# Optimization experiments

Hardware: AMD Instinct MI355X
Metric: run time of the kernel (lower is better)

The kernel has to match this reference:

```python
import jax, jax.numpy as jnp
import numpy as np

T, P, E, H = 200000, 100000, 600000, 256

def setup_inputs() -> dict:
    key = jax.random.key(0)
    ks = jax.random.split(key, 8)
    x = jax.random.normal(ks[0], (T, H), dtype=jnp.float32)
    points = jax.random.normal(ks[1], (P, 3), dtype=jnp.float32)
    triangles = jax.random.randint(ks[2], (T, 3), 0, P)
    triangle_edges = jax.random.randint(ks[3], (2, E), 0, T)
    din = H + 9
    W1 = jax.random.normal(ks[4], (din, H), dtype=jnp.float32) / np.sqrt(din)
    b1 = jnp.zeros((H,), dtype=jnp.float32)
    W2 = jax.random.normal(ks[5], (H, H), dtype=jnp.float32) / np.sqrt(H)
    b2 = jnp.zeros((H,), dtype=jnp.float32)
    return {"x": x, "points": points, "triangles": triangles,
            "triangle_edges": triangle_edges, "W1": W1, "b1": b1, "W2": W2, "b2": b2}

def reference(x, points, triangles, triangle_edges, W1, b1, W2, b2):
    # Per-triangle geometry: [T, 3(corners), 3(xyz)]
    tp = points[triangles]
    e_ij = tp[:, 0] - tp[:, 1]
    e_ik = tp[:, 0] - tp[:, 2]
    e_jk = tp[:, 1] - tp[:, 2]
    edge_vectors = jnp.stack([e_ij, e_ik, e_jk], axis=1)  # [T,3,3]
    t_max = jnp.max(edge_vectors, axis=1).astype(x.dtype)  # [T,3]
    t_min = jnp.min(edge_vectors, axis=1).astype(x.dtype)  # [T,3]
    barycenters = jnp.mean(tp, axis=1).astype(x.dtype)     # [T,3]

    src = triangle_edges[0]
    tgt = triangle_edges[1]
    # Relative geometric descriptor per edge: [E, 9]
    r_n_k = jnp.concatenate([t_min[src] - t_min[tgt],
                             t_max[src] - t_max[tgt],
                             barycenters[src] - barycenters[tgt]], axis=1)
    feature_diff = x[src] - x[tgt]                          # [E, H]
    mlp_in = jnp.concatenate([r_n_k, feature_diff], axis=1)  # [E, H+9]
    h = jax.nn.relu(mlp_in @ W1 + b1)
    mlp_out = h @ W2 + b2                                   # [E, H]
    # Scatter-add back to source triangles (order-independent sum)
    new_features = jax.ops.segment_sum(mlp_out, src, num_segments=x.shape[0])
    return new_features.astype(x.dtype)
```

## Files before the change

kernel.cpp:

```cpp
#include <hip/hip_runtime.h>
#include <stdint.h>

typedef float f32x4v __attribute__((ext_vector_type(4)));
typedef short short8v __attribute__((ext_vector_type(8)));

__device__ __forceinline__ float bf2f(unsigned short u) {
  union { uint32_t i; float f; } v; v.i = ((uint32_t)u) << 16; return v.f;
}
__device__ __forceinline__ unsigned short f2bf(float f) {
  union { float f; uint32_t i; } v; v.f = f;
  uint32_t x = v.i;
  uint32_t r = (x + 0x7FFFu + ((x >> 16) & 1u)) >> 16;
  return (unsigned short)r;
}

__global__ void prep_weights(const float* __restrict__ W1, const float* __restrict__ W2,
                             unsigned short* __restrict__ W1fT, unsigned short* __restrict__ W2T) {
  int i = blockIdx.x * blockDim.x + threadIdx.x;
  if (i < 256 * 288) {
    int n = i / 288, k = i % 288;
    float v = 0.f;
    if (k < 256) v = W1[(9 + k) * 256 + n];
    else if (k < 265) v = W1[(k - 256) * 256 + n];
    W1fT[i] = f2bf(v);
// ... 81 lines not shown
  int wbase = 0;
#pragma unroll
  for (int w = 0; w < 4; ++w) if (w < wave) wbase += wsums[w];
  if (tid < nb) blockbase[tid] = wbase + inclv - v;
}

__global__ void scan3_kernel(const int* __restrict__ count, const int* __restrict__ incl,
                             const int* __restrict__ blockbase, int* __restrict__ offsets,
                             int* __restrict__ cursor, int T) {
  int idx = blockIdx.x * 1024 + threadIdx.x * 4;
  int bb = blockbase[blockIdx.x];
#pragma unroll
  for (int j = 0; j < 4; ++j) {
    int i = idx + j;
    if (i < T) {
      int o = incl[i] + bb;
      offsets[i + 1] = o;
      cursor[i] = o - count[i];
    }
  }
  if (blockIdx.x == 0 && threadIdx.x == 0) offsets[0] = 0;
}

__global__ void fill_kernel(const int* __restrict__ te, int* __restrict__ cursor,
                            int* __restrict__ tgt_list, int E) {
  int e = blockIdx.x * blockDim.x + threadIdx.x;
  if (e < E) {
    int s = te[e];
    int pos = atomicAdd(&cursor[s], 1);
    tgt_list[pos] = te[E + e];
  }
}

__launch_bounds__(256)
__global__ void ugemm_kernel(const float* __restrict__ x, const float* __restrict__ geo12,
                             const unsigned short* __restrict__ W1fT,
                             unsigned short* __restrict__ U, int T) {
  __shared__ alignas(16) unsigned short Al[2][64][40];
  int m0 = blockIdx.x * 64;
  int tid = threadIdx.x;
  int wid = tid >> 6, lane = tid & 63;
  int srow = tid >> 2, cq = tid & 3;
  int l15 = lane & 15, lhi = lane >> 4;
  int nbase = wid * 64;
  f32x4v acc[4][4] = {};
  const unsigned short* bp[4];
#pragma unroll
  for (int nf = 0; nf < 4; ++nf)
    bp[nf] = W1fT + (size_t)(nbase + nf * 16 + l15) * 288 + 8 * lhi;
  int t = m0 + srow;

  auto loadf = [&](int kk, float* f) {
    if (kk < 8) {
      const float* sp = x + (size_t)t * 256 + kk * 32 + cq * 8;
      float4 a = *(const float4*)sp;
      float4 b = *(const float4*)(sp + 4);
      f[0] = a.x; f[1] = a.y; f[2] = a.z; f[3] = a.w;
      f[4] = b.x; f[5] = b.y; f[6] = b.z; f[7] = b.w;
    } else {
      if (cq == 0) {
        float4 a = *(const float4*)(geo12 + (size_t)t * 12);
        float4 b = *(const float4*)(geo12 + (size_t)t * 12 + 4);
        f[0] = a.x; f[1] = a.y; f[2] = a.z; f[3] = a.w;
        f[4] = b.x; f[5] = b.y; f[6] = b.z; f[7] = b.w;
      } else if (cq == 1) {
        float4 a = *(const float4*)(geo12 + (size_t)t * 12 + 8);
        f[0] = a.x; f[1] = a.y; f[2] = a.z; f[3] = a.w;
        f[4] = 0.f; f[5] = 0.f; f[6] = 0.f; f[7] = 0.f;
      } else {
        f[0] = f[1] = f[2] = f[3] = f[4] = f[5] = f[6] = f[7] = 0.f;
      }
    }
  };

  {
    float f[8];
    loadf(0, f);
    short8v av;
#pragma unroll
    for (int j = 0; j < 8; ++j) av[j] = (short)f2bf(f[j]);
    *(short8v*)(&Al[0][srow][cq * 8]) = av;
  }
  __syncthreads();

  for (int kk = 0; kk < 9; ++kk) {
    int cur = kk & 1;
    float fn[8];
    if (kk < 8) loadf(kk + 1, fn);
    short8v a[4];
#pragma unroll
    for (int mi = 0; mi < 4; ++mi)
      a[mi] = *(const short8v*)(&Al[cur][mi * 16 + l15][8 * lhi]);
#pragma unroll
    for (int nf = 0; nf < 4; ++nf) {
      short8v b = *(const short8v*)(bp[nf] + kk * 32);
#pragma unroll
      for (int mi = 0; mi < 4; ++mi)
        acc[mi][nf] = __builtin_amdgcn_mfma_f32_16x16x32_bf16(a[mi], b, acc[mi][nf], 0, 0, 0);
    }
    if (kk < 8) {
      short8v av;
#pragma unroll
      for (int j = 0; j < 8; ++j) av[j] = (short)f2bf(fn[j]);
      *(short8v*)(&Al[cur ^ 1][srow][cq * 8]) = av;
    }
    __syncthreads();
  }
#pragma unroll
  for (int mi = 0; mi < 4; ++mi) {
#pragma unroll
    for (int i = 0; i < 4; ++i) {
      int m = m0 + mi * 16 + 4 * lhi + i;
#pragma unroll
      for (int nf = 0; nf < 4; ++nf) {
        int n = nbase + nf * 16 + l15;
        U[(size_t)m * 256 + n] = f2bf(acc[mi][nf][i]);
      }
    }
  }
}

__launch_bounds__(512, 4)
__global__ void fused_kernel(const unsigned short* __restrict__ U,
                             const unsigned short* __restrict__ W2T,
                             const int* __restrict__ offsets,
                             const int* __restrict__ count,
                             const int* __restrict__ tgt_list,
                             const float* __restrict__ b1,
                             const float* __restrict__ b2,
                             float* __restrict__ out, int T) {
  __shared__ alignas(16) unsigned short hl[32][264];
  int t0 = blockIdx.x * 32;
  int tid = threadIdx.x;
  int rA = tid >> 5;
  int rB = rA + 16;
  int c8 = (tid & 31) * 8;
  {
    int tA = t0 + rA, tB = t0 + rB;
    int begA = offsets[tA], endA = offsets[tA + 1];
    int begB = offsets[tB], endB = offsets[tB + 1];
    float b1r[8];
    {
      float4 a = *(const float4*)(b1 + c8);
      float4 b = *(const float4*)(b1 + c8 + 4);
      b1r[0] = a.x; b1r[1] = a.y; b1r[2] = a.z; b1r[3] = a.w;
      b1r[4] = b.x; b1r[5] = b.y; b1r[6] = b.z; b1r[7] = b.w;
    }
    short8v uva = *(const short8v*)(U + (size_t)tA * 256 + c8);
    short8v uvb = *(const short8v*)(U + (size_t)tB * 256 + c8);
    float uA[8], sA[8], uB[8], sB[8];
#pragma unroll
    for (int j = 0; j < 8; ++j) {
      uA[j] = bf2f((unsigned short)uva[j]) + b1r[j]; sA[j] = 0.f;
      uB[j] = bf2f((unsigned short)uvb[j]) + b1r[j]; sB[j] = 0.f;
    }
    int eiA = begA, eiB = begB;
    while (eiA < endA || eiB < endB) {
      bool hasA = eiA < endA, hasB = eiB < endB;
      int laA = hasA ? endA - 1 : 0;
      int laB = hasB ? endB - 1 : 0;
      int a0 = hasA ? eiA : 0;
      int a1 = hasA ? min(eiA + 1, laA) : 0;
      int a2 = hasA ? min(eiA + 2, laA) : 0;
      int a3 = hasA ? min(eiA + 3, laA) : 0;
      int b0 = hasB ? eiB : 0;
      int b1i = hasB ? min(eiB + 1, laB) : 0;
      int b2i = hasB ? min(eiB + 2, laB) : 0;
      int b3 = hasB ? min(eiB + 3, laB) : 0;
      int gA0 = tgt_list[a0], gA1 = tgt_list[a1], gA2 = tgt_list[a2], gA3 = tgt_list[a3];
      int gB0 = tgt_list[b0], gB1 = tgt_list[b1i], gB2 = tgt_list[b2i], gB3 = tgt_list[b3];
      short8v vA0 = *(const short8v*)(U + (size_t)gA0 * 256 + c8);
      short8v vA1 = *(const short8v*)(U + (size_t)gA1 * 256 + c8);
      short8v vA2 = *(const short8v*)(U + (size_t)gA2 * 256 + c8);
      short8v vA3 = *(const short8v*)(U + (size_t)gA3 * 256 + c8);
      short8v vB0 = *(const short8v*)(U + (size_t)gB0 * 256 + c8);
      short8v vB1 = *(const short8v*)(U + (size_t)gB1 * 256 + c8);
      short8v vB2 = *(const short8v*)(U + (size_t)gB2 * 256 + c8);
      short8v vB3 = *(const short8v*)(U + (size_t)gB3 * 256 + c8);
      float mA0 = hasA ? 1.f : 0.f;
      float mA1 = (hasA && eiA + 1 <= laA) ? 1.f : 0.f;
      float mA2 = (hasA && eiA + 2 <= laA) ? 1.f : 0.f;
      float mA3 = (hasA && eiA + 3 <= laA) ? 1.f : 0.f;
      float mB0 = hasB ? 1.f : 0.f;
      float mB1 = (hasB && eiB + 1 <= laB) ? 1.f : 0.f;
      float mB2 = (hasB && eiB + 2 <= laB) ? 1.f : 0.f;
      float mB3 = (hasB && eiB + 3 <= laB) ? 1.f : 0.f;
#pragma unroll
      for (int j = 0; j < 8; ++j) {
        sA[j] += mA0 * fmaxf(uA[j] - bf2f((unsigned short)vA0[j]), 0.f)
               + mA1 * fmaxf(uA[j] - bf2f((unsigned short)vA1[j]), 0.f)
               + mA2 * fmaxf(uA[j] - bf2f((unsigned short)vA2[j]), 0.f)
               + mA3 * fmaxf(uA[j] - bf2f((unsigned short)vA3[j]), 0.f);
        sB[j] += mB0 * fmaxf(uB[j] - bf2f((unsigned short)vB0[j]), 0.f)
               + mB1 * fmaxf(uB[j] - bf2f((unsigned short)vB1[j]), 0.f)
               + mB2 * fmaxf(uB[j] - bf2f((unsigned short)vB2[j]), 0.f)
               + mB3 * fmaxf(uB[j] - bf2f((unsigned short)vB3[j]), 0.f);
      }
      if (hasA) eiA += 4;
      if (hasB) eiB += 4;
    }
    short8v hva, hvb;
#pragma unroll
    for (int j = 0; j < 8; ++j) { hva[j] = (short)f2bf(sA[j]); hvb[j] = (short)f2bf(sB[j]); }
    *(short8v*)(&hl[rA][c8]) = hva;
    *(short8v*)(&hl[rB][c8]) = hvb;
  }
  __syncthreads();
  int wid = tid >> 6, lane = tid & 63;
  int l15 = lane & 15, lhi = lane >> 4;
  int nbase = wid * 32;
  f32x4v acc[2][2] = {};
  const unsigned short* bp[2];
  float b2r[2];
#pragma unroll
  for (int nf = 0; nf < 2; ++nf) {
    bp[nf] = W2T + (size_t)(nbase + nf * 16 + l15) * 256 + 8 * lhi;
    b2r[nf] = b2[nbase + nf * 16 + l15];
  }
  for (int kk = 0; kk < 8; ++kk) {
    int k0 = kk * 32;
    short8v a0 = *(const short8v*)(&hl[l15][k0 + 8 * lhi]);
    short8v a1 = *(const short8v*)(&hl[16 + l15][k0 + 8 * lhi]);
#pragma unroll
    for (int nf = 0; nf < 2; ++nf) {
      short8v bv = *(const short8v*)(bp[nf] + k0);
      acc[0][nf] = __builtin_amdgcn_mfma_f32_16x16x32_bf16(a0, bv, acc[0][nf], 0, 0, 0);
      acc[1][nf] = __builtin_amdgcn_mfma_f32_16x16x32_bf16(a1, bv, acc[1][nf], 0, 0, 0);
    }
  }
#pragma unroll
  for (int mi = 0; mi < 2; ++mi) {
#pragma unroll
    for (int i = 0; i < 4; ++i) {
      int t = t0 + mi * 16 + 4 * lhi + i;
      float cnt = (float)count[t];
#pragma unroll
      for (int nf = 0; nf < 2; ++nf) {
        int n = nbase + nf * 16 + l15;
        out[(size_t)t * 256 + n] = acc[mi][nf][i] + cnt * b2r[nf];
      }
    }
  }
}

extern "C" void kernel_launch(void* const* d_in, const int* in_sizes, int n_in,
                              void* d_out, int out_size, void* d_ws, size_t ws_size,
                              hipStream_t stream) {
  const float* x = (const float*)d_in[0];
  const float* points = (const float*)d_in[1];
  const int* triangles = (const int*)d_in[2];
  const int* te = (const int*)d_in[3];
  const float* W1 = (const float*)d_in[4];
  const float* b1 = (const float*)d_in[5];
  const float* W2 = (const float*)d_in[6];
  const float* b2 = (const float*)d_in[7];
  float* out = (float*)d_out;
  int T = in_sizes[0] / 256;
  int E = in_sizes[3] / 2;

  char* ws = (char*)d_ws;
  size_t off = 0;
  auto alloc = [&](size_t bytes) {
    void* p = ws + off;
    off = (off + bytes + 255) & ~(size_t)255;
    return p;
  };
  unsigned short* U     = (unsigned short*)alloc((size_t)T * 256 * 2);
  float*          geo12 = (float*)alloc((size_t)T * 12 * 4);
  unsigned short* W1fT  = (unsigned short*)alloc((size_t)256 * 288 * 2);
  unsigned short* W2T   = (unsigned short*)alloc((size_t)256 * 256 * 2);
  int* count   = (int*)alloc((size_t)T * 4);
  int* offsets = (int*)alloc((size_t)(T + 1) * 4);
  int* cursor  = (int*)alloc((size_t)T * 4);
  int* tgtl    = (int*)alloc((size_t)E * 4);
  int* incl    = (int*)alloc((size_t)T * 4);
  int* bsum    = (int*)alloc(256 * 4);
  int* bbase   = (int*)alloc(256 * 4);
  if (off > ws_size) return;

  int nb1 = (T + 1023) / 1024;
  hipMemsetAsync(count, 0, (size_t)T * 4, stream);
  prep_weights<<<288, 256, 0, stream>>>(W1, W2, W1fT, W2T);
  geo_kernel<<<(T + 255) / 256, 256, 0, stream>>>(points, triangles, geo12, T);
  count_kernel<<<(E + 255) / 256, 256, 0, stream>>>(te, count, E);
  scan1_kernel<<<nb1, 256, 0, stream>>>(count, incl, bsum, T);
  scan2_kernel<<<1, 256, 0, stream>>>(bsum, bbase, nb1);
  scan3_kernel<<<nb1, 256, 0, stream>>>(count, incl, bbase, offsets, cursor, T);
  fill_kernel<<<(E + 255) / 256, 256, 0, stream>>>(te, cursor, tgtl, E);
  ugemm_kernel<<<(T + 63) / 64, 256, 0, stream>>>(x, geo12, W1fT, U, T);
  fused_kernel<<<(T + 31) / 32, 512, 0, stream>>>(U, W2T, offsets, count, tgtl, b1, b2, out, T);
}
```

Measured before the change: 364.3 us.

## Split fused gather+GEMM kernel into separate gather and output GEMM kernels

Replaces the fused kernel, which gathered neighbour rows, applied ReLU and ran the W2 GEMM in one pass, with two kernels. A gather kernel assigns one 32-thread group per triangle, loads four neighbours per iteration and writes the summed hidden activations as bf16. A separate MFMA GEMM kernel then multiplies by W2 and adds count*b2. The split separates the latency-bound irregular gather from the compute-bound GEMM so each can use its own occupancy and launch shape. The cost is an extra T×256 bf16 round trip through global memory and one more launch, and the old fused path is kept as a fallback when the workspace is too small.

```diff
diff --git a/kernel.cpp b/kernel.cpp
--- a/kernel.cpp
+++ b/kernel.cpp
@@ -220,6 +220,111 @@
       for (int nf = 0; nf < 4; ++nf) {
         int n = nbase + nf * 16 + l15;
         U[(size_t)m * 256 + n] = f2bf(acc[mi][nf][i]);
+      }
+    }
+  }
+}
+
+__launch_bounds__(256, 6)
+__global__ void gather_kernel(const unsigned short* __restrict__ U,
+                              const int* __restrict__ offsets,
+                              const int* __restrict__ tgt_list,
+                              const float* __restrict__ b1,
+                              unsigned short* __restrict__ sum_h, int T) {
+  int gid = blockIdx.x * blockDim.x + threadIdx.x;
+  int t = gid >> 5;
+  if (t >= T) return;
+  int c8 = (gid & 31) * 8;
+  int beg = offsets[t], end = offsets[t + 1];
+  short8v uvv = *(const short8v*)(U + (size_t)t * 256 + c8);
+  float4 ba = *(const float4*)(b1 + c8);
+  float4 bb = *(const float4*)(b1 + c8 + 4);
+  float u[8], s[8];
+  u[0] = bf2f((unsigned short)uvv[0]) + ba.x; u[1] = bf2f((unsigned short)uvv[1]) + ba.y;
+  u[2] = bf2f((unsigned short)uvv[2]) + ba.z; u[3] = bf2f((unsigned short)uvv[3]) + ba.w;
+  u[4] = bf2f((unsigned short)uvv[4]) + bb.x; u[5] = bf2f((unsigned short)uvv[5]) + bb.y;
+  u[6] = bf2f((unsigned short)uvv[6]) + bb.z; u[7] = bf2f((unsigned short)uvv[7]) + bb.w;
+#pragma unroll
+  for (int j = 0; j < 8; ++j) s[j] = 0.f;
+  for (int ei = beg; ei < end; ei += 4) {
+    int last = end - 1;
+    int i1 = (ei + 1 <= last) ? ei + 1 : last;
+    int i2 = (ei + 2 <= last) ? ei + 2 : last;
+    int i3 = (ei + 3 <= last) ? ei + 3 : last;
+    int g0 = tgt_list[ei], g1 = tgt_list[i1], g2 = tgt_list[i2], g3 = tgt_list[i3];
+    short8v v0 = *(const short8v*)(U + (size_t)g0 * 256 + c8);
+    short8v v1 = *(const short8v*)(U + (size_t)g1 * 256 + c8);
+    short8v v2 = *(const short8v*)(U + (size_t)g2 * 256 + c8);
+    short8v v3 = *(const short8v*)(U + (size_t)g3 * 256 + c8);
+    float m1 = (ei + 1 <= last) ? 1.f : 0.f;
+    float m2 = (ei + 2 <= last) ? 1.f : 0.f;
+    float m3 = (ei + 3 <= last) ? 1.f : 0.f;
+#pragma unroll
+    for (int j = 0; j < 8; ++j) {
+      s[j] += fmaxf(u[j] - bf2f((unsigned short)v0[j]), 0.f)
+            + m1 * fmaxf(u[j] - bf2f((unsigned short)v1[j]), 0.f)
+            + m2 * fmaxf(u[j] - bf2f((unsigned short)v2[j]), 0.f)
+            + m3 * fmaxf(u[j] - bf2f((unsigned short)v3[j]), 0.f);
+    }
+  }
+  short8v hv;
+#pragma unroll
+  for (int j = 0; j < 8; ++j) hv[j] = (short)f2bf(s[j]);
+  *(short8v*)(sum_h + (size_t)t * 256 + c8) = hv;
+}
+
+__launch_bounds__(256)
+__global__ void out_gemm_kernel(const unsigned short* __restrict__ sum_h,
+                                const unsigned short* __restrict__ W2T,
+                                const int* __restrict__ count,
+                                const float* __restrict__ b2,
+                                float* __restrict__ out, int T) {
+  __shared__ alignas(16) unsigned short Al[2][64][40];
+  int m0 = blockIdx.x * 64;
+  int tid = threadIdx.x;
+  int wid = tid >> 6, lane = tid & 63;
+  int srow = tid >> 2, cq = tid & 3;
+  int l15 = lane & 15, lhi = lane >> 4;
+  int nbase = wid * 64;
+  f32x4v acc[4][4] = {};
+  const unsigned short* bp[4];
+  float b2r[4];
+#pragma unroll
+  for (int nf = 0; nf < 4; ++nf) {
+    bp[nf] = W2T + (size_t)(nbase + nf * 16 + l15) * 256 + 8 * lhi;
+    b2r[nf] = b2[nbase + nf * 16 + l15];
+  }
+  const unsigned short* ap = sum_h + (size_t)(m0 + srow) * 256 + cq * 8;
+  *(short8v*)(&Al[0][srow][cq * 8]) = *(const short8v*)ap;
+  __syncthreads();
+  for (int kk = 0; kk < 8; ++kk) {
+    int cur = kk & 1;
+    short8v pre;
+    if (kk < 7) pre = *(const short8v*)(ap + (kk + 1) * 32);
+    short8v a[4];
+#pragma unroll
+    for (int mi = 0; mi < 4; ++mi)
+      a[mi] = *(const short8v*)(&Al[cur][mi * 16 + l15][8 * lhi]);
+#pragma unroll
+    for (int nf = 0; nf < 4; ++nf) {
+      short8v b = *(const short8v*)(bp[nf] + kk * 32);
+#pragma unroll
+      for (int mi = 0; mi < 4; ++mi)
+        acc[mi][nf] = __builtin_amdgcn_mfma_f32_16x16x32_bf16(a[mi], b, acc[mi][nf], 0, 0, 0);
+    }
+    if (kk < 7) *(short8v*)(&Al[cur ^ 1][srow][cq * 8]) = pre;
+    __syncthreads();
+  }
+#pragma unroll
+  for (int mi = 0; mi < 4; ++mi) {
+#pragma unroll
+    for (int i = 0; i < 4; ++i) {
+      int t = m0 + mi * 16 + 4 * lhi + i;
+      float cnt = (float)count[t];
+#pragma unroll
+      for (int nf = 0; nf < 4; ++nf) {
+        int n = nbase + nf * 16 + l15;
+        out[(size_t)t * 256 + n] = acc[mi][nf][i] + cnt * b2r[nf];
       }
     }
   }
@@ -381,7 +486,10 @@
   int* incl    = (int*)alloc((size_t)T * 4);
   int* bsum    = (int*)alloc(256 * 4);
   int* bbase   = (int*)alloc(256 * 4);
-  if (off > ws_size) return;
+  size_t base_off = off;
+  unsigned short* sum_h = (unsigned short*)alloc((size_t)T * 256 * 2);
+  bool split = (off <= ws_size);
+  if (base_off > ws_size) return;
 
   int nb1 = (T + 1023) / 1024;
   hipMemsetAsync(count, 0, (size_t)T * 4, stream);
@@ -393,5 +501,10 @@
   scan3_kernel<<<nb1, 256, 0, stream>>>(count, incl, bbase, offsets, cursor, T);
   fill_kernel<<<(E + 255) / 256, 256, 0, stream>>>(te, cursor, tgtl, E);
   ugemm_kernel<<<(T + 63) / 64, 256, 0, stream>>>(x, geo12, W1fT, U, T);
-  fused_kernel<<<(T + 31) / 32, 512, 0, stream>>>(U, W2T, offsets, count, tgtl, b1, b2, out, T);
-}
+  if (split) {
+    gather_kernel<<<(T * 32 + 255) / 256, 256, 0, stream>>>(U, offsets, tgtl, b1, sum_h, T);
+    out_gemm_kernel<<<(T + 63) / 64, 256, 0, stream>>>(sum_h, W2T, count, b2, out, T);
+  } else {
+    fused_kernel<<<(T + 31) / 32, 512, 0, stream>>>(U, W2T, offsets, count, tgtl, b1, b2, out, T);
+  }
+}
```

New measurement: 363.5 us. Within noise of the previous version (-0.2%).

## Split fused gather+GEMM into separate gather and 64-row output GEMM kernels

Applied to the files above, without the earlier changes.

Splits the fused gather-and-MLP kernel into a standalone gather kernel that writes per-triangle ReLU sums (bf16) to a new workspace buffer, and a separate 64x256-tile MFMA GEMM kernel for the W2 projection. The gather kernel pairs triangles t and t+T/2 per thread group, and the first GEMM now stages K in chunks of 64 instead of 32, halving its barrier count. This trades an extra round trip of a T x 256 bf16 buffer through memory for a higher-occupancy gather and better tensor-core reuse in the output GEMM.

```diff
diff --git a/kernel.cpp b/kernel.cpp
--- a/kernel.cpp
+++ b/kernel.cpp
@@ -141,7 +141,7 @@
 __global__ void ugemm_kernel(const float* __restrict__ x, const float* __restrict__ geo12,
                              const unsigned short* __restrict__ W1fT,
                              unsigned short* __restrict__ U, int T) {
-  __shared__ alignas(16) unsigned short Al[2][64][40];
+  __shared__ alignas(16) unsigned short Al[2][64][72];
   int m0 = blockIdx.x * 64;
   int tid = threadIdx.x;
   int wid = tid >> 6, lane = tid & 63;
@@ -154,62 +154,82 @@
   for (int nf = 0; nf < 4; ++nf)
     bp[nf] = W1fT + (size_t)(nbase + nf * 16 + l15) * 288 + 8 * lhi;
   int t = m0 + srow;
-
-  auto loadf = [&](int kk, float* f) {
-    if (kk < 8) {
-      const float* sp = x + (size_t)t * 256 + kk * 32 + cq * 8;
-      float4 a = *(const float4*)sp;
-      float4 b = *(const float4*)(sp + 4);
+  const float* xrow = x + (size_t)t * 256 + cq * 16;
+
+  auto loadx = [&](int kk, float* f) {
+    const float* sp = xrow + kk * 64;
+#pragma unroll
+    for (int q = 0; q < 4; ++q) {
+      float4 a = *(const float4*)(sp + q * 4);
+      f[q * 4 + 0] = a.x; f[q * 4 + 1] = a.y; f[q * 4 + 2] = a.z; f[q * 4 + 3] = a.w;
+    }
+  };
+  auto storeA = [&](int buf, float* f) {
+    short8v v0, v1;
+#pragma unroll
+    for (int j = 0; j < 8; ++j) { v0[j] = (short)f2bf(f[j]); v1[j] = (short)f2bf(f[8 + j]); }
+    *(short8v*)(&Al[buf][srow][cq * 16]) = v0;
+    *(short8v*)(&Al[buf][srow][cq * 16 + 8]) = v1;
+  };
+
+  {
+    float f[16];
+    loadx(0, f);
+    storeA(0, f);
+  }
+  __syncthreads();
+
+  for (int kk = 0; kk < 4; ++kk) {
+    int cur = kk & 1;
+    float fn[16];
+    if (kk < 3) loadx(kk + 1, fn);
+#pragma unroll
+    for (int k2 = 0; k2 < 2; ++k2) {
+      short8v a[4];
+#pragma unroll
+      for (int mi = 0; mi < 4; ++mi)
+        a[mi] = *(const short8v*)(&Al[cur][mi * 16 + l15][k2 * 32 + 8 * lhi]);
+#pragma unroll
+      for (int nf = 0; nf < 4; ++nf) {
+        short8v b = *(const short8v*)(bp[nf] + kk * 64 + k2 * 32);
+#pragma unroll
+        for (int mi = 0; mi < 4; ++mi)
+          acc[mi][nf] = __builtin_amdgcn_mfma_f32_16x16x32_bf16(a[mi], b, acc[mi][nf], 0, 0, 0);
+      }
+    }
+    if (kk < 3) storeA(cur ^ 1, fn);
+    __syncthreads();
+  }
+  {
+    float f[8];
+    if (cq == 0) {
+      float4 a = *(const float4*)(geo12 + (size_t)t * 12);
+      float4 b = *(const float4*)(geo12 + (size_t)t * 12 + 4);
       f[0] = a.x; f[1] = a.y; f[2] = a.z; f[3] = a.w;
       f[4] = b.x; f[5] = b.y; f[6] = b.z; f[7] = b.w;
+    } else if (cq == 1) {
+      float4 a = *(const float4*)(geo12 + (size_t)t * 12 + 8);
+      f[0] = a.x; f[1] = a.y; f[2] = a.z; f[3] = a.w;
+      f[4] = 0.f; f[5] = 0.f; f[6] = 0.f; f[7] = 0.f;
     } else {
-      if (cq == 0) {
-        float4 a = *(const float4*)(geo12 + (size_t)t * 12);
-        float4 b = *(const float4*)(geo12 + (size_t)t * 12 + 4);
-        f[0] = a.x; f[1] = a.y; f[2] = a.z; f[3] = a.w;
-        f[4] = b.x; f[5] = b.y; f[6] = b.z; f[7] = b.w;
-      } else if (cq == 1) {
-        float4 a = *(const float4*)(geo12 + (size_t)t * 12 + 8);
-        f[0] = a.x; f[1] = a.y; f[2] = a.z; f[3] = a.w;
-        f[4] = 0.f; f[5] = 0.f; f[6] = 0.f; f[7] = 0.f;
-      } else {
-        f[0] = f[1] = f[2] = f[3] = f[4] = f[5] = f[6] = f[7] = 0.f;
-      }
-    }
-  };
-
-  {
-    float f[8];
-    loadf(0, f);
+      f[0] = f[1] = f[2] = f[3] = f[4] = f[5] = f[6] = f[7] = 0.f;
+    }
     short8v av;
 #pragma unroll
     for (int j = 0; j < 8; ++j) av[j] = (short)f2bf(f[j]);
     *(short8v*)(&Al[0][srow][cq * 8]) = av;
-  }
-  __syncthreads();
-
-  for (int kk = 0; kk < 9; ++kk) {
-    int cur = kk & 1;
-    float fn[8];
-    if (kk < 8) loadf(kk + 1, fn);
+    __syncthreads();
     short8v a[4];
 #pragma unroll
     for (int mi = 0; mi < 4; ++mi)
-      a[mi] = *(const short8v*)(&Al[cur][mi * 16 + l15][8 * lhi]);
+      a[mi] = *(const short8v*)(&Al[0][mi * 16 + l15][8 * lhi]);
 #pragma unroll
     for (int nf = 0; nf < 4; ++nf) {
-      short8v b = *(const short8v*)(bp[nf] + kk * 32);
+      short8v b = *(const short8v*)(bp[nf] + 256);
 #pragma unroll
       for (int mi = 0; mi < 4; ++mi)
         acc[mi][nf] = __builtin_amdgcn_mfma_f32_16x16x32_bf16(a[mi], b, acc[mi][nf], 0, 0, 0);
     }
-    if (kk < 8) {
-      short8v av;
-#pragma unroll
-      for (int j = 0; j < 8; ++j) av[j] = (short)f2bf(fn[j]);
-      *(short8v*)(&Al[cur ^ 1][srow][cq * 8]) = av;
-    }
-    __syncthreads();
   }
 #pragma unroll
   for (int mi = 0; mi < 4; ++mi) {
@@ -225,122 +245,152 @@
   }
 }
 
-__launch_bounds__(512, 4)
-__global__ void fused_kernel(const unsigned short* __restrict__ U,
-                             const unsigned short* __restrict__ W2T,
-                             const int* __restrict__ offsets,
-                             const int* __restrict__ count,
-                             const int* __restrict__ tgt_list,
-                             const float* __restrict__ b1,
-                             const float* __restrict__ b2,
-                             float* __restrict__ out, int T) {
-  __shared__ alignas(16) unsigned short hl[32][264];
-  int t0 = blockIdx.x * 32;
+__launch_bounds__(256, 4)
+__global__ void gather_kernel(const unsigned short* __restrict__ U,
+                              const int* __restrict__ offsets,
+                              const int* __restrict__ tgt_list,
+                              const float* __restrict__ b1,
+                              unsigned short* __restrict__ sum_h, int T) {
+  int gid = blockIdx.x * blockDim.x + threadIdx.x;
+  int half = (T + 1) >> 1;
+  int pair = gid >> 5;
+  if (pair >= half) return;
+  int c8 = (gid & 31) * 8;
+  int tA = pair, tB = pair + half;
+  bool hasRowB = tB < T;
+  int begA = offsets[tA], endA = offsets[tA + 1];
+  int begB = hasRowB ? offsets[tB] : 0, endB = hasRowB ? offsets[tB + 1] : 0;
+  float b1r[8];
+  {
+    float4 a = *(const float4*)(b1 + c8);
+    float4 b = *(const float4*)(b1 + c8 + 4);
+    b1r[0] = a.x; b1r[1] = a.y; b1r[2] = a.z; b1r[3] = a.w;
+    b1r[4] = b.x; b1r[5] = b.y; b1r[6] = b.z; b1r[7] = b.w;
+  }
+  short8v uva = *(const short8v*)(U + (size_t)tA * 256 + c8);
+  short8v uvb = *(const short8v*)(U + (size_t)(hasRowB ? tB : tA) * 256 + c8);
+  float uA[8], sA[8], uB[8], sB[8];
+#pragma unroll
+  for (int j = 0; j < 8; ++j) {
+    uA[j] = bf2f((unsigned short)uva[j]) + b1r[j]; sA[j] = 0.f;
+    uB[j] = bf2f((unsigned short)uvb[j]) + b1r[j]; sB[j] = 0.f;
+  }
+  int eiA = begA, eiB = begB;
+  while (eiA < endA || eiB < endB) {
+    bool hasA = eiA < endA, hasB = eiB < endB;
+    int laA = hasA ? endA - 1 : 0;
+    int laB = hasB ? endB - 1 : 0;
+    int a0 = hasA ? eiA : 0;
+    int a1 = hasA ? min(eiA + 1, laA) : 0;
+    int a2 = hasA ? min(eiA + 2, laA) : 0;
+    int a3 = hasA ? min(eiA + 3, laA) : 0;
+    int b0 = hasB ? eiB : 0;
+    int b1i = hasB ? min(eiB + 1, laB) : 0;
+    int b2i = hasB ? min(eiB + 2, laB) : 0;
+    int b3 = hasB ? min(eiB + 3, laB) : 0;
+    int gA0 = tgt_list[a0], gA1 = tgt_list[a1], gA2 = tgt_list[a2], gA3 = tgt_list[a3];
+    int gB0 = tgt_list[b0], gB1 = tgt_list[b1i], gB2 = tgt_list[b2i], gB3 = tgt_list[b3];
+    short8v vA0 = *(const short8v*)(U + (size_t)gA0 * 256 + c8);
+    short8v vA1 = *(const short8v*)(U + (size_t)gA1 * 256 + c8);
+    short8v vA2 = *(const short8v*)(U + (size_t)gA2 * 256 + c8);
+    short8v vA3 = *(const short8v*)(U + (size_t)gA3 * 256 + c8);
+    short8v vB0 = *(const short8v*)(U + (size_t)gB0 * 256 + c8);
+    short8v vB1 = *(const short8v*)(U + (size_t)gB1 * 256 + c8);
+    short8v vB2 = *(const short8v*)(U + (size_t)gB2 * 256 + c8);
+    short8v vB3 = *(const short8v*)(U + (size_t)gB3 * 256 + c8);
+    float mA0 = hasA ? 1.f : 0.f;
+    float mA1 = (hasA && eiA + 1 <= laA) ? 1.f : 0.f;
+    float mA2 = (hasA && eiA + 2 <= laA) ? 1.f : 0.f;
+    float mA3 = (hasA && eiA + 3 <= laA) ? 1.f : 0.f;
+    float mB0 = hasB ? 1.f : 0.f;
+    float mB1 = (hasB && eiB + 1 <= laB) ? 1.f : 0.f;
+    float mB2 = (hasB && eiB + 2 <= laB) ? 1.f : 0.f;
+    float mB3 = (hasB && eiB + 3 <= laB) ? 1.f : 0.f;
+#pragma unroll
+    for (int j = 0; j < 8; ++j) {
+      sA[j] += mA0 * fmaxf(uA[j] - bf2f((unsigned short)vA0[j]), 0.f)
+             + mA1 * fmaxf(uA[j] - bf2f((unsigned short)vA1[j]), 0.f)
+             + mA2 * fmaxf(uA[j] - bf2f((unsigned short)vA2[j]), 0.f)
+             + mA3 * fmaxf(uA[j] - bf2f((unsigned short)vA3[j]), 0.f);
+      sB[j] += mB0 * fmaxf(uB[j] - bf2f((unsigned short)vB0[j]), 0.f)
+             + mB1 * fmaxf(uB[j] - bf2f((unsigned short)vB1[j]), 0.f)
+             + mB2 * fmaxf(uB[j] - bf2f((unsigned short)vB2[j]), 0.f)
+             + mB3 * fmaxf(uB[j] - bf2f((unsigned short)vB3[j]), 0.f);
+    }
+    if (hasA) eiA += 4;
+    if (hasB) eiB += 4;
+  }
+  short8v hva, hvb;
+#pragma unroll
+  for (int j = 0; j < 8; ++j) { hva[j] = (short)f2bf(sA[j]); hvb[j] = (short)f2bf(sB[j]); }
+  *(short8v*)(sum_h + (size_t)tA * 256 + c8) = hva;
+  if (hasRowB) *(short8v*)(sum_h + (size_t)tB * 256 + c8) = hvb;
+}
+
+__launch_bounds__(256)
+__global__ void out_gemm_kernel(const unsigned short* __restrict__ sum_h,
+                                const unsigned short* __restrict__ W2T,
+                                const int* __restrict__ count,
+                                const float* __restrict__ b2,
+                                float* __restrict__ out, int T) {
+  __shared__ alignas(16) unsigned short Al[2][64][72];
+  int m0 = blockIdx.x * 64;
   int tid = threadIdx.x;
-  int rA = tid >> 5;
-  int rB = rA + 16;
-  int c8 = (tid & 31) * 8;
-  {
-    int tA = t0 + rA, tB = t0 + rB;
-    int begA = offsets[tA], endA = offsets[tA + 1];
-    int begB = offsets[tB], endB = offsets[tB + 1];
-    float b1r[8];
-    {
-      float4 a = *(const float4*)(b1 + c8);
-      float4 b = *(const float4*)(b1 + c8 + 4);
-      b1r[0] = a.x; b1r[1] = a.y; b1r[2] = a.z; b1r[3] = a.w;
-      b1r[4] = b.x; b1r[5] = b.y; b1r[6] = b.z; b1r[7] = b.w;
-    }
-    short8v uva = *(const short8v*)(U + (size_t)tA * 256 + c8);
-    short8v uvb = *(const short8v*)(U + (size_t)tB * 256 + c8);
-    float uA[8], sA[8], uB[8], sB[8];
-#pragma unroll
-    for (int j = 0; j < 8; ++j) {
-      uA[j] = bf2f((unsigned short)uva[j]) + b1r[j]; sA[j] = 0.f;
-      uB[j] = bf2f((unsigned short)uvb[j]) + b1r[j]; sB[j] = 0.f;
-    }
-    int eiA = begA, eiB = begB;
-    while (eiA < endA || eiB < endB) {
-      bool hasA = eiA < endA, hasB = eiB < endB;
-      int laA = hasA ? endA - 1 : 0;
-      int laB = hasB ? endB - 1 : 0;
-      int a0 = hasA ? eiA : 0;
-      int a1 = hasA ? min(eiA + 1, laA) : 0;
-      int a2 = hasA ? min(eiA + 2, laA) : 0;
-      int a3 = hasA ? min(eiA + 3, laA) : 0;
-      int b0 = hasB ? eiB : 0;
-      int b1i = hasB ? min(eiB + 1, laB) : 0;
-      int b2i = hasB ? min(eiB + 2, laB) : 0;
-      int b3 = hasB ? min(eiB + 3, laB) : 0;
-      int gA0 = tgt_list[a0], gA1 = tgt_list[a1], gA2 = tgt_list[a2], gA3 = tgt_list[a3];
-      int gB0 = tgt_list[b0], gB1 = tgt_list[b1i], gB2 = tgt_list[b2i], gB3 = tgt_list[b3];
-      short8v vA0 = *(const short8v*)(U + (size_t)gA0 * 256 + c8);
-      short8v vA1 = *(const short8v*)(U + (size_t)gA1 * 256 + c8);
-      short8v vA2 = *(const short8v*)(U + (size_t)gA2 * 256 + c8);
-      short8v vA3 = *(const short8v*)(U + (size_t)gA3 * 256 + c8);
-      short8v vB0 = *(const short8v*)(U + (size_t)gB0 * 256 + c8);
-      short8v vB1 = *(const short8v*)(U + (size_t)gB1 * 256 + c8);
-      short8v vB2 = *(const short8v*)(U + (size_t)gB2 * 256 + c8);
-      short8v vB3 = *(const short8v*)(U + (size_t)gB3 * 256 + c8);
-      float mA0 = hasA ? 1.f : 0.f;
-      float mA1 = (hasA && eiA + 1 <= laA) ? 1.f : 0.f;
-      float mA2 = (hasA && eiA + 2 <= laA) ? 1.f : 0.f;
-      float mA3 = (hasA && eiA + 3 <= laA) ? 1.f : 0.f;
-      float mB0 = hasB ? 1.f : 0.f;
-      float mB1 = (hasB && eiB + 1 <= laB) ? 1.f : 0.f;
-      float mB2 = (hasB && eiB + 2 <= laB) ? 1.f : 0.f;
-      float mB3 = (hasB && eiB + 3 <= laB) ? 1.f : 0.f;
-#pragma unroll
-      for (int j = 0; j < 8; ++j) {
-        sA[j] += mA0 * fmaxf(uA[j] - bf2f((unsigned short)vA0[j]), 0.f)
-               + mA1 * fmaxf(uA[j] - bf2f((unsigned short)vA1[j]), 0.f)
-               + mA2 * fmaxf(uA[j] - bf2f((unsigned short)vA2[j]), 0.f)
-               + mA3 * fmaxf(uA[j] - bf2f((unsigned short)vA3[j]), 0.f);
-        sB[j] += mB0 * fmaxf(uB[j] - bf2f((unsigned short)vB0[j]), 0.f)
-               + mB1 * fmaxf(uB[j] - bf2f((unsigned short)vB1[j]), 0.f)
-               + mB2 * fmaxf(uB[j] - bf2f((unsigned short)vB2[j]), 0.f)
-               + mB3 * fmaxf(uB[j] - bf2f((unsigned short)vB3[j]), 0.f);
-      }
-      if (hasA) eiA += 4;
-      if (hasB) eiB += 4;
-    }
-    short8v hva, hvb;
-#pragma unroll
-    for (int j = 0; j < 8; ++j) { hva[j] = (short)f2bf(sA[j]); hvb[j] = (short)f2bf(sB[j]); }
-    *(short8v*)(&hl[rA][c8]) = hva;
-    *(short8v*)(&hl[rB][c8]) = hvb;
-  }
-  __syncthreads();
   int wid = tid >> 6, lane = tid & 63;
+  int srow = tid >> 2, cq = tid & 3;
   int l15 = lane & 15, lhi = lane >> 4;
-  int nbase = wid * 32;
-  f32x4v acc[2][2] = {};
-  const unsigned short* bp[2];
-  float b2r[2];
-#pragma unroll
-  for (int nf = 0; nf < 2; ++nf) {
+  int nbase = wid * 64;
+  f32x4v acc[4][4] = {};
+  const unsigned short* bp[4];
+  float b2r[4];
+#pragma unroll
+  for (int nf = 0; nf < 4; ++nf) {
     bp[nf] = W2T + (size_t)(nbase + nf * 16 + l15) * 256 + 8 * lhi;
     b2r[nf] = b2[nbase + nf * 16 + l15];
   }
-  for (int kk = 0; kk < 8; ++kk) {
-    int k0 = kk * 32;
-    short8v a0 = *(const short8v*)(&hl[l15][k0 + 8 * lhi]);
-    short8v a1 = *(const short8v*)(&hl[16 + l15][k0 + 8 * lhi]);
-#pragma unroll
-    for (int nf = 0; nf < 2; ++nf) {
-      short8v bv = *(const short8v*)(bp[nf] + k0);
-      acc[0][nf] = __builtin_amdgcn_mfma_f32_16x16x32_bf16(a0, bv, acc[0][nf], 0, 0, 0);
-      acc[1][nf] = __builtin_amdgcn_mfma_f32_16x16x32_bf16(a1, bv, acc[1][nf], 0, 0, 0);
-    }
-  }
-#pragma unroll
-  for (int mi = 0; mi < 2; ++mi) {
+  const unsigned short* ap = sum_h + (size_t)(m0 + srow) * 256 + cq * 16;
+  {
+    short8v v0 = *(const short8v*)ap;
+    short8v v1 = *(const short8v*)(ap + 8);
+    *(short8v*)(&Al[0][srow][cq * 16]) = v0;
+    *(short8v*)(&Al[0][srow][cq * 16 + 8]) = v1;
+  }
+  __syncthreads();
+  for (int kk = 0; kk < 4; ++kk) {
+    int cur = kk & 1;
+    short8v p0, p1;
+    if (kk < 3) {
+      p0 = *(const short8v*)(ap + (kk + 1) * 64);
+      p1 = *(const short8v*)(ap + (kk + 1) * 64 + 8);
+    }
+#pragma unroll
+    for (int k2 = 0; k2 < 2; ++k2) {
+      short8v a[4];
+#pragma unroll
+      for (int mi = 0; mi < 4; ++mi)
+        a[mi] = *(const short8v*)(&Al[cur][mi * 16 + l15][k2 * 32 + 8 * lhi]);
+#pragma unroll
+      for (int nf = 0; nf < 4; ++nf) {
+        short8v b = *(const short8v*)(bp[nf] + kk * 64 + k2 * 32);
+#pragma unroll
+        for (int mi = 0; mi < 4; ++mi)
+          acc[mi][nf] = __builtin_amdgcn_mfma_f32_16x16x32_bf16(a[mi], b, acc[mi][nf], 0, 0, 0);
+      }
+    }
+    if (kk < 3) {
+      *(short8v*)(&Al[cur ^ 1][srow][cq * 16]) = p0;
+      *(short8v*)(&Al[cur ^ 1][srow][cq * 16 + 8]) = p1;
+    }
+    __syncthreads();
+  }
+#pragma unroll
+  for (int mi = 0; mi < 4; ++mi) {
 #pragma unroll
     for (int i = 0; i < 4; ++i) {
-      int t = t0 + mi * 16 + 4 * lhi + i;
+      int t = m0 + mi * 16 + 4 * lhi + i;
       float cnt = (float)count[t];
 #pragma unroll
-      for (int nf = 0; nf < 2; ++nf) {
+      for (int nf = 0; nf < 4; ++nf) {
         int n = nbase + nf * 16 + l15;
         out[(size_t)t * 256 + n] = acc[mi][nf][i] + cnt * b2r[nf];
       }
@@ -381,6 +431,7 @@
   int* incl    = (int*)alloc((size_t)T * 4);
   int* bsum    = (int*)alloc(256 * 4);
   int* bbase   = (int*)alloc(256 * 4);
+  unsigned short* sum_h = (unsigned short*)alloc((size_t)T * 256 * 2);
   if (off > ws_size) return;
 
   int nb1 = (T + 1023) / 1024;
@@ -393,5 +444,9 @@
   scan3_kernel<<<nb1, 256, 0, stream>>>(count, incl, bbase, offsets, cursor, T);
   fill_kernel<<<(E + 255) / 256, 256, 0, stream>>>(te, cursor, tgtl, E);
   ugemm_kernel<<<(T + 63) / 64, 256, 0, stream>>>(x, geo12, W1fT, U, T);
-  fused_kernel<<<(T + 31) / 32, 512, 0, stream>>>(U, W2T, offsets, count, tgtl, b1, b2, out, T);
-}
+  {
+    int half = (T + 1) >> 1;
+    gather_kernel<<<(half * 32 + 255) / 256, 256, 0, stream>>>(U, offsets, tgtl, b1, sum_h, T);
+  }
+  out_gemm_kernel<<<(T + 63) / 64, 256, 0, stream>>>(sum_h, W2T, count, b2, out, T);
+}
```

Result: slower. 375.6 us (+3.1%).

## Split fused gather+GEMM into separate gather and per-wave output GEMM kernels

Applied to the files above, without the earlier changes.

Replaces the fused gather-then-W2-GEMM kernel with a standalone gather kernel that writes summed hidden activations to a bf16 workspace, followed by a separate output GEMM kernel. Both GEMMs are rewritten to have each wave compute a 16x128 tile, reading A directly from global memory with no LDS staging and no block barriers. The gather pairs rows t and t+T/2 instead of adjacent rows. The aim is higher occupancy and no barrier stalls in exchange for an extra T×256 bf16 write and read round trip.

```diff
diff --git a/kernel.cpp b/kernel.cpp
--- a/kernel.cpp
+++ b/kernel.cpp
@@ -137,213 +137,184 @@
   }
 }
 
-__launch_bounds__(256)
+__launch_bounds__(256, 4)
 __global__ void ugemm_kernel(const float* __restrict__ x, const float* __restrict__ geo12,
                              const unsigned short* __restrict__ W1fT,
                              unsigned short* __restrict__ U, int T) {
-  __shared__ alignas(16) unsigned short Al[2][64][40];
-  int m0 = blockIdx.x * 64;
-  int tid = threadIdx.x;
-  int wid = tid >> 6, lane = tid & 63;
-  int srow = tid >> 2, cq = tid & 3;
+  int wg = (blockIdx.x * 256 + threadIdx.x) >> 6;
+  int lane = threadIdx.x & 63;
   int l15 = lane & 15, lhi = lane >> 4;
-  int nbase = wid * 64;
-  f32x4v acc[4][4] = {};
-  const unsigned short* bp[4];
-#pragma unroll
-  for (int nf = 0; nf < 4; ++nf)
-    bp[nf] = W1fT + (size_t)(nbase + nf * 16 + l15) * 288 + 8 * lhi;
-  int t = m0 + srow;
-
-  auto loadf = [&](int kk, float* f) {
-    if (kk < 8) {
-      const float* sp = x + (size_t)t * 256 + kk * 32 + cq * 8;
-      float4 a = *(const float4*)sp;
-      float4 b = *(const float4*)(sp + 4);
-      f[0] = a.x; f[1] = a.y; f[2] = a.z; f[3] = a.w;
-      f[4] = b.x; f[5] = b.y; f[6] = b.z; f[7] = b.w;
+  int strip = wg >> 1;
+  int nbase = (wg & 1) * 128;
+  if (strip * 16 >= T) return;
+  int row = strip * 16 + l15;
+  const float* xrow = x + (size_t)row * 256 + 8 * lhi;
+  const unsigned short* bp = W1fT + (size_t)(nbase + l15) * 288 + 8 * lhi;
+  f32x4v acc[8] = {};
+#pragma unroll 2
+  for (int kk = 0; kk < 8; ++kk) {
+    float4 a0 = *(const float4*)(xrow + kk * 32);
+    float4 a1 = *(const float4*)(xrow + kk * 32 + 4);
+    short8v av;
+    av[0] = (short)f2bf(a0.x); av[1] = (short)f2bf(a0.y);
+    av[2] = (short)f2bf(a0.z); av[3] = (short)f2bf(a0.w);
+    av[4] = (short)f2bf(a1.x); av[5] = (short)f2bf(a1.y);
+    av[6] = (short)f2bf(a1.z); av[7] = (short)f2bf(a1.w);
+#pragma unroll
+    for (int nf = 0; nf < 8; ++nf) {
+      short8v bv = *(const short8v*)(bp + (size_t)nf * 4608 + kk * 32);
+      acc[nf] = __builtin_amdgcn_mfma_f32_16x16x32_bf16(av, bv, acc[nf], 0, 0, 0);
+    }
+  }
+  {
+    float g[8];
+    if (lhi == 0) {
+      float4 a = *(const float4*)(geo12 + (size_t)row * 12);
+      float4 b = *(const float4*)(geo12 + (size_t)row * 12 + 4);
+      g[0] = a.x; g[1] = a.y; g[2] = a.z; g[3] = a.w;
+      g[4] = b.x; g[5] = b.y; g[6] = b.z; g[7] = b.w;
+    } else if (lhi == 1) {
+      float4 a = *(const float4*)(geo12 + (size_t)row * 12 + 8);
+      g[0] = a.x; g[1] = a.y; g[2] = a.z; g[3] = a.w;
+      g[4] = 0.f; g[5] = 0.f; g[6] = 0.f; g[7] = 0.f;
     } else {
-      if (cq == 0) {
-        float4 a = *(const float4*)(geo12 + (size_t)t * 12);
-        float4 b = *(const float4*)(geo12 + (size_t)t * 12 + 4);
-        f[0] = a.x; f[1] = a.y; f[2] = a.z; f[3] = a.w;
-        f[4] = b.x; f[5] = b.y; f[6] = b.z; f[7] = b.w;
-      } else if (cq == 1) {
-        float4 a = *(const float4*)(geo12 + (size_t)t * 12 + 8);
-        f[0] = a.x; f[1] = a.y; f[2] = a.z; f[3] = a.w;
-        f[4] = 0.f; f[5] = 0.f; f[6] = 0.f; f[7] = 0.f;
-      } else {
-        f[0] = f[1] = f[2] = f[3] = f[4] = f[5] = f[6] = f[7] = 0.f;
-      }
-    }
-  };
-
+      g[0] = g[1] = g[2] = g[3] = g[4] = g[5] = g[6] = g[7] = 0.f;
+    }
+    short8v av;
+#pragma unroll
+    for (int j = 0; j < 8; ++j) av[j] = (short)f2bf(g[j]);
+#pragma unroll
+    for (int nf = 0; nf < 8; ++nf) {
+      short8v bv = *(const short8v*)(bp + (size_t)nf * 4608 + 256);
+      acc[nf] = __builtin_amdgcn_mfma_f32_16x16x32_bf16(av, bv, acc[nf], 0, 0, 0);
+    }
+  }
+#pragma unroll
+  for (int i = 0; i < 4; ++i) {
+    int m = strip * 16 + 4 * lhi + i;
+#pragma unroll
+    for (int nf = 0; nf < 8; ++nf) {
+      int n = nbase + nf * 16 + l15;
+      U[(size_t)m * 256 + n] = f2bf(acc[nf][i]);
+    }
+  }
+}
+
+__launch_bounds__(256, 4)
+__global__ void gather_kernel(const unsigned short* __restrict__ U,
+                              const int* __restrict__ offsets,
+                              const int* __restrict__ tgt_list,
+                              const float* __restrict__ b1,
+                              unsigned short* __restrict__ sum_h, int T) {
+  int gid = blockIdx.x * blockDim.x + threadIdx.x;
+  int half = (T + 1) >> 1;
+  int pair = gid >> 5;
+  if (pair >= half) return;
+  int c8 = (gid & 31) * 8;
+  int tA = pair, tB = pair + half;
+  bool hasRowB = tB < T;
+  int begA = offsets[tA], endA = offsets[tA + 1];
+  int begB = hasRowB ? offsets[tB] : 0, endB = hasRowB ? offsets[tB + 1] : 0;
+  float b1r[8];
   {
-    float f[8];
-    loadf(0, f);
-    short8v av;
-#pragma unroll
-    for (int j = 0; j < 8; ++j) av[j] = (short)f2bf(f[j]);
-    *(short8v*)(&Al[0][srow][cq * 8]) = av;
-  }
-  __syncthreads();
-
-  for (int kk = 0; kk < 9; ++kk) {
-    int cur = kk & 1;
-    float fn[8];
-    if (kk < 8) loadf(kk + 1, fn);
-    short8v a[4];
-#pragma unroll
-    for (int mi = 0; mi < 4; ++mi)
-      a[mi] = *(const short8v*)(&Al[cur][mi * 16 + l15][8 * lhi]);
-#pragma unroll
-    for (int nf = 0; nf < 4; ++nf) {
-      short8v b = *(const short8v*)(bp[nf] + kk * 32);
-#pragma unroll
-      for (int mi = 0; mi < 4; ++mi)
-        acc[mi][nf] = __builtin_amdgcn_mfma_f32_16x16x32_bf16(a[mi], b, acc[mi][nf], 0, 0, 0);
-    }
-    if (kk < 8) {
-      short8v av;
-#pragma unroll
-      for (int j = 0; j < 8; ++j) av[j] = (short)f2bf(fn[j]);
-      *(short8v*)(&Al[cur ^ 1][srow][cq * 8]) = av;
-    }
-    __syncthreads();
-  }
-#pragma unroll
-  for (int mi = 0; mi < 4; ++mi) {
-#pragma unroll
-    for (int i = 0; i < 4; ++i) {
-      int m = m0 + mi * 16 + 4 * lhi + i;
-#pragma unroll
-      for (int nf = 0; nf < 4; ++nf) {
-        int n = nbase + nf * 16 + l15;
-        U[(size_t)m * 256 + n] = f2bf(acc[mi][nf][i]);
-      }
-    }
-  }
-}
-
-__launch_bounds__(512, 4)
-__global__ void fused_kernel(const unsigned short* __restrict__ U,
-                             const unsigned short* __restrict__ W2T,
-                             const int* __restrict__ offsets,
-                             const int* __restrict__ count,
-                             const int* __restrict__ tgt_list,
-                             const float* __restrict__ b1,
-                             const float* __restrict__ b2,
-                             float* __restrict__ out, int T) {
-  __shared__ alignas(16) unsigned short hl[32][264];
-  int t0 = blockIdx.x * 32;
-  int tid = threadIdx.x;
-  int rA = tid >> 5;
-  int rB = rA + 16;
-  int c8 = (tid & 31) * 8;
-  {
-    int tA = t0 + rA, tB = t0 + rB;
-    int begA = offsets[tA], endA = offsets[tA + 1];
-    int begB = offsets[tB], endB = offsets[tB + 1];
-    float b1r[8];
-    {
-      float4 a = *(const float4*)(b1 + c8);
-      float4 b = *(const float4*)(b1 + c8 + 4);
-      b1r[0] = a.x; b1r[1] = a.y; b1r[2] = a.z; b1r[3] = a.w;
-      b1r[4] = b.x; b1r[5] = b.y; b1r[6] = b.z; b1r[7] = b.w;
-    }
-    short8v uva = *(const short8v*)(U + (size_t)tA * 256 + c8);
-    short8v uvb = *(const short8v*)(U + (size_t)tB * 256 + c8);
-    float uA[8], sA[8], uB[8], sB[8];
+    float4 a = *(const float4*)(b1 + c8);
+    float4 b = *(const float4*)(b1 + c8 + 4);
+    b1r[0] = a.x; b1r[1] = a.y; b1r[2] = a.z; b1r[3] = a.w;
+    b1r[4] = b.x; b1r[5] = b.y; b1r[6] = b.z; b1r[7] = b.w;
+  }
+  short8v uva = *(const short8v*)(U + (size_t)tA * 256 + c8);
+  short8v uvb = *(const short8v*)(U + (size_t)(hasRowB ? tB : tA) * 256 + c8);
+  float uA[8], sA[8], uB[8], sB[8];
+#pragma unroll
+  for (int j = 0; j < 8; ++j) {
+    uA[j] = bf2f((unsigned short)uva[j]) + b1r[j]; sA[j] = 0.f;
+    uB[j] = bf2f((unsigned short)uvb[j]) + b1r[j]; sB[j] = 0.f;
+  }
+  int eiA = begA, eiB = begB;
+  while (eiA < endA || eiB < endB) {
+    bool hasA = eiA < endA, hasB = eiB < endB;
+    int laA = hasA ? endA - 1 : 0;
+    int laB = hasB ? endB - 1 : 0;
+    int a0 = hasA ? eiA : 0;
+    int a1 = hasA ? min(eiA + 1, laA) : 0;
+    int a2 = hasA ? min(eiA + 2, laA) : 0;
+    int a3 = hasA ? min(eiA + 3, laA) : 0;
+    int b0 = hasB ? eiB : 0;
+    int b1i = hasB ? min(eiB + 1, laB) : 0;
+    int b2i = hasB ? min(eiB + 2, laB) : 0;
+    int b3 = hasB ? min(eiB + 3, laB) : 0;
+    int gA0 = tgt_list[a0], gA1 = tgt_list[a1], gA2 = tgt_list[a2], gA3 = tgt_list[a3];
+    int gB0 = tgt_list[b0], gB1 = tgt_list[b1i], gB2 = tgt_list[b2i], gB3 = tgt_list[b3];
+    short8v vA0 = *(const short8v*)(U + (size_t)gA0 * 256 + c8);
+    short8v vA1 = *(const short8v*)(U + (size_t)gA1 * 256 + c8);
+    short8v vA2 = *(const short8v*)(U + (size_t)gA2 * 256 + c8);
+    short8v vA3 = *(const short8v*)(U + (size_t)gA3 * 256 + c8);
+    short8v vB0 = *(const short8v*)(U + (size_t)gB0 * 256 + c8);
+    short8v vB1 = *(const short8v*)(U + (size_t)gB1 * 256 + c8);
+    short8v vB2 = *(const short8v*)(U + (size_t)gB2 * 256 + c8);
+    short8v vB3 = *(const short8v*)(U + (size_t)gB3 * 256 + c8);
+    float mA0 = hasA ? 1.f : 0.f;
+    float mA1 = (hasA && eiA + 1 <= laA) ? 1.f : 0.f;
+    float mA2 = (hasA && eiA + 2 <= laA) ? 1.f : 0.f;
+    float mA3 = (hasA && eiA + 3 <= laA) ? 1.f : 0.f;
+    float mB0 = hasB ? 1.f : 0.f;
+    float mB1 = (hasB && eiB + 1 <= laB) ? 1.f : 0.f;
+    float mB2 = (hasB && eiB + 2 <= laB) ? 1.f : 0.f;
+    float mB3 = (hasB && eiB + 3 <= laB) ? 1.f : 0.f;
 #pragma unroll
     for (int j = 0; j < 8; ++j) {
-      uA[j] = bf2f((unsigned short)uva[j]) + b1r[j]; sA[j] = 0.f;
-      uB[j] = bf2f((unsigned short)uvb[j]) + b1r[j]; sB[j] = 0.f;
-    }
-    int eiA = begA, eiB = begB;
-    while (eiA < endA || eiB < endB) {
-      bool hasA = eiA < endA, hasB = eiB < endB;
-      int laA = hasA ? endA - 1 : 0;
-      int laB = hasB ? endB - 1 : 0;
-      int a0 = hasA ? eiA : 0;
-      int a1 = hasA ? min(eiA + 1, laA) : 0;
-      int a2 = hasA ? min(eiA + 2, laA) : 0;
-      int a3 = hasA ? min(eiA + 3, laA) : 0;
-      int b0 = hasB ? eiB : 0;
-      int b1i = hasB ? min(eiB + 1, laB) : 0;
-      int b2i = hasB ? min(eiB + 2, laB) : 0;
-      int b3 = hasB ? min(eiB + 3, laB) : 0;
-      int gA0 = tgt_list[a0], gA1 = tgt_list[a1], gA2 = tgt_list[a2], gA3 = tgt_list[a3];
-      int gB0 = tgt_list[b0], gB1 = tgt_list[b1i], gB2 = tgt_list[b2i], gB3 = tgt_list[b3];
-      short8v vA0 = *(const short8v*)(U + (size_t)gA0 * 256 + c8);
-      short8v vA1 = *(const short8v*)(U + (size_t)gA1 * 256 + c8);
-      short8v vA2 = *(const short8v*)(U + (size_t)gA2 * 256 + c8);
-      short8v vA3 = *(const short8v*)(U + (size_t)gA3 * 256 + c8);
-      short8v vB0 = *(const short8v*)(U + (size_t)gB0 * 256 + c8);
-      short8v vB1 = *(const short8v*)(U + (size_t)gB1 * 256 + c8);
-      short8v vB2 = *(const short8v*)(U + (size_t)gB2 * 256 + c8);
-      short8v vB3 = *(const short8v*)(U + (size_t)gB3 * 256 + c8);
-      float mA0 = hasA ? 1.f : 0.f;
-      float mA1 = (hasA && eiA + 1 <= laA) ? 1.f : 0.f;
-      float mA2 = (hasA && eiA + 2 <= laA) ? 1.f : 0.f;
-      float mA3 = (hasA && eiA + 3 <= laA) ? 1.f : 0.f;
-      float mB0 = hasB ? 1.f : 0.f;
-      float mB1 = (hasB && eiB + 1 <= laB) ? 1.f : 0.f;
-      float mB2 = (hasB && eiB + 2 <= laB) ? 1.f : 0.f;
-      float mB3 = (hasB && eiB + 3 <= laB) ? 1.f : 0.f;
-#pragma unroll
-      for (int j = 0; j < 8; ++j) {
-        sA[j] += mA0 * fmaxf(uA[j] - bf2f((unsigned short)vA0[j]), 0.f)
-               + mA1 * fmaxf(uA[j] - bf2f((unsigned short)vA1[j]), 0.f)
-               + mA2 * fmaxf(uA[j] - bf2f((unsigned short)vA2[j]), 0.f)
-               + mA3 * fmaxf(uA[j] - bf2f((unsigned short)vA3[j]), 0.f);
-        sB[j] += mB0 * fmaxf(uB[j] - bf2f((unsigned short)vB0[j]), 0.f)
-               + mB1 * fmaxf(uB[j] - bf2f((unsigned short)vB1[j]), 0.f)
-               + mB2 * fmaxf(uB[j] - bf2f((unsigned short)vB2[j]), 0.f)
-               + mB3 * fmaxf(uB[j] - bf2f((unsigned short)vB3[j]), 0.f);
-      }
-      if (hasA) eiA += 4;
-      if (hasB) eiB += 4;
-    }
-    short8v hva, hvb;
-#pragma unroll
-    for (int j = 0; j < 8; ++j) { hva[j] = (short)f2bf(sA[j]); hvb[j] = (short)f2bf(sB[j]); }
-    *(short8v*)(&hl[rA][c8]) = hva;
-    *(short8v*)(&hl[rB][c8]) = hvb;
-  }
-  __syncthreads();
-  int wid = tid >> 6, lane = tid & 63;
+      sA[j] += mA0 * fmaxf(uA[j] - bf2f((unsigned short)vA0[j]), 0.f)
+             + mA1 * fmaxf(uA[j] - bf2f((unsigned short)vA1[j]), 0.f)
+             + mA2 * fmaxf(uA[j] - bf2f((unsigned short)vA2[j]), 0.f)
+             + mA3 * fmaxf(uA[j] - bf2f((unsigned short)vA3[j]), 0.f);
+      sB[j] += mB0 * fmaxf(uB[j] - bf2f((unsigned short)vB0[j]), 0.f)
+             + mB1 * fmaxf(uB[j] - bf2f((unsigned short)vB1[j]), 0.f)
+             + mB2 * fmaxf(uB[j] - bf2f((unsigned short)vB2[j]), 0.f)
+             + mB3 * fmaxf(uB[j] - bf2f((unsigned short)vB3[j]), 0.f);
+    }
+    if (hasA) eiA += 4;
+    if (hasB) eiB += 4;
+  }
+  short8v hva, hvb;
+#pragma unroll
+  for (int j = 0; j < 8; ++j) { hva[j] = (short)f2bf(sA[j]); hvb[j] = (short)f2bf(sB[j]); }
+  *(short8v*)(sum_h + (size_t)tA * 256 + c8) = hva;
+  if (hasRowB) *(short8v*)(sum_h + (size_t)tB * 256 + c8) = hvb;
+}
+
+__launch_bounds__(256, 4)
+__global__ void out_gemm_kernel(const unsigned short* __restrict__ sum_h,
+                                const unsigned short* __restrict__ W2T,
+                                const int* __restrict__ count,
+                                const float* __restrict__ b2,
+                                float* __restrict__ out, int T) {
+  int wg = (blockIdx.x * 256 + threadIdx.x) >> 6;
+  int lane = threadIdx.x & 63;
   int l15 = lane & 15, lhi = lane >> 4;
-  int nbase = wid * 32;
-  f32x4v acc[2][2] = {};
-  const unsigned short* bp[2];
-  float b2r[2];
-#pragma unroll
-  for (int nf = 0; nf < 2; ++nf) {
-    bp[nf] = W2T + (size_t)(nbase + nf * 16 + l15) * 256 + 8 * lhi;
-    b2r[nf] = b2[nbase + nf * 16 + l15];
-  }
+  int strip = wg >> 1;
+  int nbase = (wg & 1) * 128;
+  if (strip * 16 >= T) return;
+  int row = strip * 16 + l15;
+  const unsigned short* arow = sum_h + (size_t)row * 256 + 8 * lhi;
+  const unsigned short* bp = W2T + (size_t)(nbase + l15) * 256 + 8 * lhi;
+  f32x4v acc[8] = {};
+#pragma unroll 2
   for (int kk = 0; kk < 8; ++kk) {
-    int k0 = kk * 32;
-    short8v a0 = *(const short8v*)(&hl[l15][k0 + 8 * lhi]);
-    short8v a1 = *(const short8v*)(&hl[16 + l15][k0 + 8 * lhi]);
-#pragma unroll
-    for (int nf = 0; nf < 2; ++nf) {
-      short8v bv = *(const short8v*)(bp[nf] + k0);
-      acc[0][nf] = __builtin_amdgcn_mfma_f32_16x16x32_bf16(a0, bv, acc[0][nf], 0, 0, 0);
-      acc[1][nf] = __builtin_amdgcn_mfma_f32_16x16x32_bf16(a1, bv, acc[1][nf], 0, 0, 0);
-    }
-  }
-#pragma unroll
-  for (int mi = 0; mi < 2; ++mi) {
-#pragma unroll
-    for (int i = 0; i < 4; ++i) {
-      int t = t0 + mi * 16 + 4 * lhi + i;
-      float cnt = (float)count[t];
-#pragma unroll
-      for (int nf = 0; nf < 2; ++nf) {
-        int n = nbase + nf * 16 + l15;
-        out[(size_t)t * 256 + n] = acc[mi][nf][i] + cnt * b2r[nf];
-      }
+    short8v av = *(const short8v*)(arow + kk * 32);
+#pragma unroll
+    for (int nf = 0; nf < 8; ++nf) {
+      short8v bv = *(const short8v*)(bp + (size_t)nf * 4096 + kk * 32);
+      acc[nf] = __builtin_amdgcn_mfma_f32_16x16x32_bf16(av, bv, acc[nf], 0, 0, 0);
+    }
+  }
+#pragma unroll
+  for (int i = 0; i < 4; ++i) {
+    int m = strip * 16 + 4 * lhi + i;
+    float cnt = (float)count[m];
+#pragma unroll
+    for (int nf = 0; nf < 8; ++nf) {
+      int n = nbase + nf * 16 + l15;
+      out[(size_t)m * 256 + n] = acc[nf][i] + cnt * b2[n];
     }
   }
 }
@@ -381,9 +352,11 @@
   int* incl    = (int*)alloc((size_t)T * 4);
   int* bsum    = (int*)alloc(256 * 4);
   int* bbase   = (int*)alloc(256 * 4);
+  unsigned short* sum_h = (unsigned short*)alloc((size_t)T * 256 * 2);
   if (off > ws_size) return;
 
   int nb1 = (T + 1023) / 1024;
+  int nstrips = (T + 15) / 16;
   hipMemsetAsync(count, 0, (size_t)T * 4, stream);
   prep_weights<<<288, 256, 0, stream>>>(W1, W2, W1fT, W2T);
   geo_kernel<<<(T + 255) / 256, 256, 0, stream>>>(points, triangles, geo12, T);
@@ -392,6 +365,10 @@
   scan2_kernel<<<1, 256, 0, stream>>>(bsum, bbase, nb1);
   scan3_kernel<<<nb1, 256, 0, stream>>>(count, incl, bbase, offsets, cursor, T);
   fill_kernel<<<(E + 255) / 256, 256, 0, stream>>>(te, cursor, tgtl, E);
-  ugemm_kernel<<<(T + 63) / 64, 256, 0, stream>>>(x, geo12, W1fT, U, T);
-  fused_kernel<<<(T + 31) / 32, 512, 0, stream>>>(U, W2T, offsets, count, tgtl, b1, b2, out, T);
-}
+  ugemm_kernel<<<(nstrips * 2 + 3) / 4, 256, 0, stream>>>(x, geo12, W1fT, U, T);
+  {
+    int half = (T + 1) >> 1;
+    gather_kernel<<<(half * 32 + 255) / 256, 256, 0, stream>>>(U, offsets, tgtl, b1, sum_h, T);
+  }
+  out_gemm_kernel<<<(nstrips * 2 + 3) / 4, 256, 0, stream>>>(sum_h, W2T, count, b2, out, T);
+}
```

Result: slower. 593.4 us (+62.9%).
